# Kernel tuning notes

Measured on AMD Instinct MI355X. Metric: run time of the kernel, lower is better.

Reference implementation:

```python
import jax, jax.numpy as jnp
import numpy as np

NUM_CLASSES = 19
C_ENET = 1.02            # ENet weighting constant
THRESH = -float(np.log(0.7))  # -log(thresh)
N_MIN = 262144           # hard-example floor (B*H*W // 16)


def setup_inputs() -> dict:
    key = jax.random.key(0)
    k1, k2 = jax.random.split(key)
    logits = jax.random.normal(k1, (8, NUM_CLASSES, 512, 1024), dtype=jnp.float32)
    labels = jax.random.randint(k2, (8, 512, 1024), 0, NUM_CLASSES, dtype=jnp.int32)
    return {"logits": logits, "labels": labels}


def reference(logits, labels):
    # ENet class weights from label histogram: w_c = 1 / ln(c + freq_c)
    flat_lab = labels.reshape(-1)
    total = flat_lab.shape[0]
    counts = jnp.bincount(flat_lab, length=NUM_CLASSES).astype(jnp.float32)
    propensity = counts / jnp.float32(total)
    class_weights = 1.0 / jnp.log(C_ENET + propensity)  # [C]

    # weighted per-pixel cross entropy (reduction='none')
    logp = jax.nn.log_softmax(logits, axis=1)                       # [B,C,H,W]
    nll = -jnp.take_along_axis(logp, labels[:, None].astype(jnp.int32), axis=1)[:, 0]  # [B,H,W]
    loss = (class_weights[labels] * nll).reshape(-1)                # [B*H*W]

    # OHEM: sort descending, keep > thresh if n_min-th loss exceeds thresh, else top n_min
    loss_sorted = jnp.sort(loss)[::-1]
    cond = loss_sorted[N_MIN] > THRESH
    idx = jnp.arange(loss_sorted.shape[0])
    mask = jnp.where(cond, loss_sorted > THRESH, idx < N_MIN).astype(loss_sorted.dtype)
    return jnp.sum(loss_sorted * mask) / jnp.sum(mask)
```

## Files before the change

### kernel.cpp

```cpp
#include <hip/hip_runtime.h>
#include <math.h>

#define NCLS   19
#define HW     (512*1024)
#define BHW    (8*HW)
#define NQ     (BHW/4)
#define KSEL   262144u
#define THRESH 0.35667494393873245f

struct Meta {
  double S;
  double sumV;
  unsigned int cntV;
  unsigned int K;
  unsigned int b1, k1, b2, k2, vbits;
  unsigned int _pad;
  unsigned int counts[32];
  float weights[32];
  unsigned int hist1[2048];
  unsigned int hist2[2048];
  unsigned int hist3[1024];
};

__global__ __launch_bounds__(256) void k_label_hist(const int* __restrict__ lab,
                                                    Meta* __restrict__ m) {
  __shared__ unsigned int h[32];
  if (threadIdx.x < 32) h[threadIdx.x] = 0u;
  __syncthreads();
  int q = blockIdx.x * 256 + threadIdx.x;
  int4 l = reinterpret_cast<const int4*>(lab)[q];
  atomicAdd(&h[l.x], 1u);
  atomicAdd(&h[l.y], 1u);
  atomicAdd(&h[l.z], 1u);
  atomicAdd(&h[l.w], 1u);
  __syncthreads();
  if (threadIdx.x < 32) {
    unsigned int c = h[threadIdx.x];
    if (c) atomicAdd(&m->counts[threadIdx.x], c);
  }
}

__global__ void k_weights(Meta* __restrict__ m) {
  int c = threadIdx.x;
  if (c < NCLS) {
    float p = (float)m->counts[c] * (1.0f / (float)BHW);
    m->weights[c] = 1.0f / logf(1.02f + p);
  }
}

__global__ __launch_bounds__(256) void k_loss(const float* __restrict__ logits,
                                              const int* __restrict__ lab,
                                              float* __restrict__ loss,
                                              Meta* __restrict__ m) {
  __shared__ float w[NCLS];
  __shared__ float  sp[4];
  __shared__ unsigned int cp[4];
  if (threadIdx.x < NCLS) w[threadIdx.x] = m->weights[threadIdx.x];
  __syncthreads();

  int q = blockIdx.x * 256 + threadIdx.x;
  int base = q << 2;
  int b  = base >> 19;
  int hw = base & (HW - 1);
  const float* lp = logits + (long)b * (NCLS * HW) + hw;
  int4 l4 = reinterpret_cast<const int4*>(lab)[q];

  float4 vals[NCLS];
#pragma unroll
  for (int c = 0; c < NCLS; ++c) {
    vals[c] = *reinterpret_cast<const float4*>(lp);
    lp += HW;
  }

  float m0 = -INFINITY, m1 = -INFINITY, m2 = -INFINITY, m3 = -INFINITY;
#pragma unroll
  for (int c = 0; c < NCLS; ++c) {
    m0 = fmaxf(m0, vals[c].x); m1 = fmaxf(m1, vals[c].y);
    m2 = fmaxf(m2, vals[c].z); m3 = fmaxf(m3, vals[c].w);
  }
  float s0 = 0.f, s1 = 0.f, s2 = 0.f, s3 = 0.f;
  float x0 = 0.f, x1 = 0.f, x2 = 0.f, x3 = 0.f;
#pragma unroll
  for (int c = 0; c < NCLS; ++c) {
    float4 v = vals[c];
    s0 += __expf(v.x - m0); s1 += __expf(v.y - m1);
    s2 += __expf(v.z - m2); s3 += __expf(v.w - m3);
    x0 = (c == l4.x) ? v.x : x0;
    x1 = (c == l4.y) ? v.y : x1;
    x2 = (c == l4.z) ? v.z : x2;
    x3 = (c == l4.w) ? v.w : x3;
  }
  float4 o;
  o.x = w[l4.x] * (m0 + logf(s0) - x0);
  o.y = w[l4.y] * (m1 + logf(s1) - x1);
  o.z = w[l4.z] * (m2 + logf(s2) - x2);
  o.w = w[l4.w] * (m3 + logf(s3) - x3);
  reinterpret_cast<float4*>(loss)[q] = o;

  float ls = 0.f; unsigned int lc = 0u;
  if (o.x > THRESH) { ls += o.x; ++lc; }
  if (o.y > THRESH) { ls += o.y; ++lc; }
  if (o.z > THRESH) { ls += o.z; ++lc; }
  if (o.w > THRESH) { ls += o.w; ++lc; }
#pragma unroll
  for (int off = 32; off > 0; off >>= 1) {
    ls += __shfl_down(ls, off);
    lc += __shfl_down(lc, off);
  }
  int wid = threadIdx.x >> 6;
  if ((threadIdx.x & 63) == 0) { sp[wid] = ls; cp[wid] = lc; }
  __syncthreads();
  if (threadIdx.x == 0) {
    float bs = sp[0] + sp[1] + sp[2] + sp[3];
    unsigned int bc = cp[0] + cp[1] + cp[2] + cp[3];
    atomicAdd(&m->S, (double)bs);
    atomicAdd(&m->K, bc);
  }
}

__global__ __launch_bounds__(256) void k_hist1(const float* __restrict__ loss,
                                               Meta* __restrict__ m) {
  __shared__ unsigned int h[2048];
  __shared__ int active;
  if (threadIdx.x == 0) active = (m->K <= KSEL) ? 1 : 0;
  for (int i = threadIdx.x; i < 2048; i += 256) h[i] = 0u;
  __syncthreads();
  if (!active) return;
  int stride = gridDim.x * 256;
  for (int q = blockIdx.x * 256 + threadIdx.x; q < NQ; q += stride) {
    float4 v = reinterpret_cast<const float4*>(loss)[q];
    atomicAdd(&h[__float_as_uint(v.x) >> 21], 1u);
    atomicAdd(&h[__float_as_uint(v.y) >> 21], 1u);
    atomicAdd(&h[__float_as_uint(v.z) >> 21], 1u);
    atomicAdd(&h[__float_as_uint(v.w) >> 21], 1u);
  }
  __syncthreads();
  for (int i = threadIdx.x; i < 2048; i += 256)
    if (h[i]) atomicAdd(&m->hist1[i], h[i]);
}

__global__ void k_sel1(Meta* __restrict__ m) {
  if (m->K > KSEL) return;
  unsigned int cum = 0;
  for (int b = 2047; b >= 0; --b) {
    unsigned int hb = m->hist1[b];
    if (cum + hb >= KSEL) { m->b1 = (unsigned)b; m->k1 = KSEL - cum; return; }
    cum += hb;
  }
}

__global__ __launch_bounds__(256) void k_hist2(const float* __restrict__ loss,
                                               Meta* __restrict__ m) {
  __shared__ unsigned int h[2048];
  __shared__ unsigned int sb1;
  __shared__ int active;
  if (threadIdx.x == 0) { active = (m->K <= KSEL) ? 1 : 0; sb1 = m->b1; }
  for (int i = threadIdx.x; i < 2048; i += 256) h[i] = 0u;
  __syncthreads();
  if (!active) return;
  unsigned int b1 = sb1;
  int stride = gridDim.x * 256;
  for (int q = blockIdx.x * 256 + threadIdx.x; q < NQ; q += stride) {
    float4 v = reinterpret_cast<const float4*>(loss)[q];
    unsigned int bx = __float_as_uint(v.x);
    unsigned int by = __float_as_uint(v.y);
    unsigned int bz = __float_as_uint(v.z);
    unsigned int bw = __float_as_uint(v.w);
    if ((bx >> 21) == b1) atomicAdd(&h[(bx >> 10) & 2047u], 1u);
    if ((by >> 21) == b1) atomicAdd(&h[(by >> 10) & 2047u], 1u);
    if ((bz >> 21) == b1) atomicAdd(&h[(bz >> 10) & 2047u], 1u);
    if ((bw >> 21) == b1) atomicAdd(&h[(bw >> 10) & 2047u], 1u);
  }
  __syncthreads();
  for (int i = threadIdx.x; i < 2048; i += 256)
    if (h[i]) atomicAdd(&m->hist2[i], h[i]);
}

__global__ void k_sel2(Meta* __restrict__ m) {
  if (m->K > KSEL) return;
  unsigned int k1 = m->k1, cum = 0;
  for (int b = 2047; b >= 0; --b) {
    unsigned int hb = m->hist2[b];
    if (cum + hb >= k1) { m->b2 = (unsigned)b; m->k2 = k1 - cum; return; }
    cum += hb;
  }
}

__global__ __launch_bounds__(256) void k_hist3(const float* __restrict__ loss,
                                               Meta* __restrict__ m) {
  __shared__ unsigned int h[1024];
  __shared__ unsigned int spre;
  __shared__ int active;
  if (threadIdx.x == 0) {
    active = (m->K <= KSEL) ? 1 : 0;
    spre = (m->b1 << 11) | m->b2;
  }
  for (int i = threadIdx.x; i < 1024; i += 256) h[i] = 0u;
  __syncthreads();
  if (!active) return;
  unsigned int pre = spre;
  int stride = gridDim.x * 256;
  for (int q = blockIdx.x * 256 + threadIdx.x; q < NQ; q += stride) {
    float4 v = reinterpret_cast<const float4*>(loss)[q];
    unsigned int bx = __float_as_uint(v.x);
    unsigned int by = __float_as_uint(v.y);
    unsigned int bz = __float_as_uint(v.z);
    unsigned int bw = __float_as_uint(v.w);
    if ((bx >> 10) == pre) atomicAdd(&h[bx & 1023u], 1u);
    if ((by >> 10) == pre) atomicAdd(&h[by & 1023u], 1u);
    if ((bz >> 10) == pre) atomicAdd(&h[bz & 1023u], 1u);
    if ((bw >> 10) == pre) atomicAdd(&h[bw & 1023u], 1u);
  }
  __syncthreads();
  for (int i = threadIdx.x; i < 1024; i += 256)
    if (h[i]) atomicAdd(&m->hist3[i], h[i]);
}

__global__ void k_sel3(Meta* __restrict__ m) {
  if (m->K > KSEL) return;
  unsigned int k2 = m->k2, cum = 0;
  for (int b = 1023; b >= 0; --b) {
    unsigned int hb = m->hist3[b];
    if (cum + hb >= k2) {
      m->vbits = (m->b1 << 21) | (m->b2 << 10) | (unsigned)b;
      return;
    }
    cum += hb;
  }
}

__global__ __launch_bounds__(256) void k_sumv(const float* __restrict__ loss,
                                              Meta* __restrict__ m) {
  __shared__ double sp[4];
  __shared__ unsigned int cp[4];
  __shared__ unsigned int svb;
  __shared__ int active;
  if (threadIdx.x == 0) { active = (m->K <= KSEL) ? 1 : 0; svb = m->vbits; }
  __syncthreads();
  if (!active) return;
  unsigned int vb = svb;
  double ls = 0.0; unsigned int lc = 0u;
  int stride = gridDim.x * 256;
  for (int q = blockIdx.x * 256 + threadIdx.x; q < NQ; q += stride) {
    float4 v = reinterpret_cast<const float4*>(loss)[q];
    if (__float_as_uint(v.x) > vb) { ls += (double)v.x; ++lc; }
    if (__float_as_uint(v.y) > vb) { ls += (double)v.y; ++lc; }
    if (__float_as_uint(v.z) > vb) { ls += (double)v.z; ++lc; }
    if (__float_as_uint(v.w) > vb) { ls += (double)v.w; ++lc; }
  }
#pragma unroll
  for (int off = 32; off > 0; off >>= 1) {
    ls += __shfl_down(ls, off);
    lc += __shfl_down(lc, off);
  }
  int wid = threadIdx.x >> 6;
  if ((threadIdx.x & 63) == 0) { sp[wid] = ls; cp[wid] = lc; }
  __syncthreads();
  if (threadIdx.x == 0) {
    atomicAdd(&m->sumV, sp[0] + sp[1] + sp[2] + sp[3]);
    atomicAdd(&m->cntV, cp[0] + cp[1] + cp[2] + cp[3]);
  }
}

__global__ void k_final(const Meta* __restrict__ m, float* __restrict__ out) {
  if (m->K > KSEL) {
    out[0] = (float)(m->S / (double)m->K);
  } else {
    float v = __uint_as_float(m->vbits);
    double top = m->sumV + (double)(KSEL - m->cntV) * (double)v;
    out[0] = (float)(top / (double)KSEL);
  }
}

extern "C" void kernel_launch(void* const* d_in, const int* in_sizes, int n_in,
                              void* d_out, int out_size, void* d_ws, size_t ws_size,
                              hipStream_t stream) {
  const float* logits = (const float*)d_in[0];
  const int*   labels = (const int*)d_in[1];
  float* out  = (float*)d_out;
  float* loss = (float*)d_ws;
  Meta*  meta = (Meta*)((char*)d_ws + (size_t)BHW * 4);

  hipMemsetAsync(meta, 0, sizeof(Meta), stream);
  k_label_hist<<<NQ / 256, 256, 0, stream>>>(labels, meta);
  k_weights  <<<1, 64, 0, stream>>>(meta);
  k_loss     <<<NQ / 256, 256, 0, stream>>>(logits, labels, loss, meta);
  k_hist1    <<<512, 256, 0, stream>>>(loss, meta);
  k_sel1     <<<1, 1, 0, stream>>>(meta);
  k_hist2    <<<512, 256, 0, stream>>>(loss, meta);
  k_sel2     <<<1, 1, 0, stream>>>(meta);
  k_hist3    <<<512, 256, 0, stream>>>(loss, meta);
  k_sel3     <<<1, 1, 0, stream>>>(meta);
  k_sumv     <<<512, 256, 0, stream>>>(loss, meta);
  k_final    <<<1, 1, 0, stream>>>(meta, out);
}
```

Baseline: 186.2 us.

## Fuse OHEM pipeline into three kernels with last-block finalization and single-block fallback

Folds the class-weight computation into the label histogram kernel with a last-block-done counter. The final mean for the common K>KSEL case is now written inside the loss kernel the same way. The four-pass radix select, previously split across many multi-block kernels, moves into one 1024-thread block fallback kernel. This removes about eight kernel launches and their serialization. The cost is that the fallback path, whenever it runs, scans 32 MB four times with only a single workgroup, which would be very slow.

Result: slower. 390.3 us (+109.7%).

```diff
diff --git a/kernel.cpp b/kernel.cpp
--- a/kernel.cpp
+++ b/kernel.cpp
@@ -5,25 +5,22 @@
 #define HW     (512*1024)
 #define BHW    (8*HW)
 #define NQ     (BHW/4)
+#define GRID_Q (NQ/256)
 #define KSEL   262144u
 #define THRESH 0.35667494393873245f
 
 struct Meta {
   double S;
-  double sumV;
-  unsigned int cntV;
   unsigned int K;
-  unsigned int b1, k1, b2, k2, vbits;
+  unsigned int done0;
+  unsigned int done1;
   unsigned int _pad;
   unsigned int counts[32];
   float weights[32];
-  unsigned int hist1[2048];
-  unsigned int hist2[2048];
-  unsigned int hist3[1024];
 };
 
-__global__ __launch_bounds__(256) void k_label_hist(const int* __restrict__ lab,
-                                                    Meta* __restrict__ m) {
+__global__ __launch_bounds__(256) void k_hist_weights(const int* __restrict__ lab,
+                                                      Meta* __restrict__ m) {
   __shared__ unsigned int h[32];
   if (threadIdx.x < 32) h[threadIdx.x] = 0u;
   __syncthreads();
@@ -38,22 +35,27 @@
     unsigned int c = h[threadIdx.x];
     if (c) atomicAdd(&m->counts[threadIdx.x], c);
   }
-}
-
-__global__ void k_weights(Meta* __restrict__ m) {
-  int c = threadIdx.x;
-  if (c < NCLS) {
-    float p = (float)m->counts[c] * (1.0f / (float)BHW);
-    m->weights[c] = 1.0f / logf(1.02f + p);
+  __syncthreads();
+  if (threadIdx.x == 0) {
+    __threadfence();
+    unsigned int done = atomicAdd(&m->done0, 1u);
+    if (done == GRID_Q - 1u) {
+      for (int c = 0; c < NCLS; ++c) {
+        unsigned int cnt = atomicAdd(&m->counts[c], 0u);
+        float p = (float)cnt * (1.0f / (float)BHW);
+        m->weights[c] = 1.0f / logf(1.02f + p);
+      }
+    }
   }
 }
 
 __global__ __launch_bounds__(256) void k_loss(const float* __restrict__ logits,
                                               const int* __restrict__ lab,
                                               float* __restrict__ loss,
-                                              Meta* __restrict__ m) {
+                                              Meta* __restrict__ m,
+                                              float* __restrict__ out) {
   __shared__ float w[NCLS];
-  __shared__ float  sp[4];
+  __shared__ float sp[4];
   __shared__ unsigned int cp[4];
   if (threadIdx.x < NCLS) w[threadIdx.x] = m->weights[threadIdx.x];
   __syncthreads();
@@ -115,19 +117,33 @@
     unsigned int bc = cp[0] + cp[1] + cp[2] + cp[3];
     atomicAdd(&m->S, (double)bs);
     atomicAdd(&m->K, bc);
-  }
-}
-
-__global__ __launch_bounds__(256) void k_hist1(const float* __restrict__ loss,
-                                               Meta* __restrict__ m) {
+    __threadfence();
+    unsigned int done = atomicAdd(&m->done1, 1u);
+    if (done == GRID_Q - 1u) {
+      double S = atomicAdd(&m->S, 0.0);
+      unsigned int K = atomicAdd(&m->K, 0u);
+      if (K > KSEL) out[0] = (float)(S / (double)K);
+    }
+  }
+}
+
+__global__ __launch_bounds__(1024) void k_fallback(const float* __restrict__ loss,
+                                                   const Meta* __restrict__ m,
+                                                   float* __restrict__ out) {
   __shared__ unsigned int h[2048];
-  __shared__ int active;
-  if (threadIdx.x == 0) active = (m->K <= KSEL) ? 1 : 0;
-  for (int i = threadIdx.x; i < 2048; i += 256) h[i] = 0u;
-  __syncthreads();
-  if (!active) return;
-  int stride = gridDim.x * 256;
-  for (int q = blockIdx.x * 256 + threadIdx.x; q < NQ; q += stride) {
+  __shared__ unsigned int sel[4];
+  __shared__ double dsp[16];
+  __shared__ unsigned int dcp[16];
+
+  unsigned int K = m->K;
+  if (K > KSEL) return;
+
+  const int T = 1024;
+  int tid = threadIdx.x;
+
+  for (int i = tid; i < 2048; i += T) h[i] = 0u;
+  __syncthreads();
+  for (int q = tid; q < NQ; q += T) {
     float4 v = reinterpret_cast<const float4*>(loss)[q];
     atomicAdd(&h[__float_as_uint(v.x) >> 21], 1u);
     atomicAdd(&h[__float_as_uint(v.y) >> 21], 1u);
@@ -135,113 +151,66 @@
     atomicAdd(&h[__float_as_uint(v.w) >> 21], 1u);
   }
   __syncthreads();
-  for (int i = threadIdx.x; i < 2048; i += 256)
-    if (h[i]) atomicAdd(&m->hist1[i], h[i]);
-}
-
-__global__ void k_sel1(Meta* __restrict__ m) {
-  if (m->K > KSEL) return;
-  unsigned int cum = 0;
-  for (int b = 2047; b >= 0; --b) {
-    unsigned int hb = m->hist1[b];
-    if (cum + hb >= KSEL) { m->b1 = (unsigned)b; m->k1 = KSEL - cum; return; }
-    cum += hb;
-  }
-}
-
-__global__ __launch_bounds__(256) void k_hist2(const float* __restrict__ loss,
-                                               Meta* __restrict__ m) {
-  __shared__ unsigned int h[2048];
-  __shared__ unsigned int sb1;
-  __shared__ int active;
-  if (threadIdx.x == 0) { active = (m->K <= KSEL) ? 1 : 0; sb1 = m->b1; }
-  for (int i = threadIdx.x; i < 2048; i += 256) h[i] = 0u;
-  __syncthreads();
-  if (!active) return;
-  unsigned int b1 = sb1;
-  int stride = gridDim.x * 256;
-  for (int q = blockIdx.x * 256 + threadIdx.x; q < NQ; q += stride) {
-    float4 v = reinterpret_cast<const float4*>(loss)[q];
-    unsigned int bx = __float_as_uint(v.x);
-    unsigned int by = __float_as_uint(v.y);
-    unsigned int bz = __float_as_uint(v.z);
-    unsigned int bw = __float_as_uint(v.w);
+  if (tid == 0) {
+    unsigned int cum = 0;
+    for (int b = 2047; b >= 0; --b) {
+      unsigned int hb = h[b];
+      if (cum + hb >= KSEL) { sel[0] = (unsigned)b; sel[3] = KSEL - cum; break; }
+      cum += hb;
+    }
+  }
+  __syncthreads();
+  unsigned int b1 = sel[0], k1 = sel[3];
+
+  for (int i = tid; i < 2048; i += T) h[i] = 0u;
+  __syncthreads();
+  for (int q = tid; q < NQ; q += T) {
+    float4 v = reinterpret_cast<const float4*>(loss)[q];
+    unsigned int bx = __float_as_uint(v.x), by = __float_as_uint(v.y);
+    unsigned int bz = __float_as_uint(v.z), bw = __float_as_uint(v.w);
     if ((bx >> 21) == b1) atomicAdd(&h[(bx >> 10) & 2047u], 1u);
     if ((by >> 21) == b1) atomicAdd(&h[(by >> 10) & 2047u], 1u);
     if ((bz >> 21) == b1) atomicAdd(&h[(bz >> 10) & 2047u], 1u);
     if ((bw >> 21) == b1) atomicAdd(&h[(bw >> 10) & 2047u], 1u);
   }
   __syncthreads();
-  for (int i = threadIdx.x; i < 2048; i += 256)
-    if (h[i]) atomicAdd(&m->hist2[i], h[i]);
-}
-
-__global__ void k_sel2(Meta* __restrict__ m) {
-  if (m->K > KSEL) return;
-  unsigned int k1 = m->k1, cum = 0;
-  for (int b = 2047; b >= 0; --b) {
-    unsigned int hb = m->hist2[b];
-    if (cum + hb >= k1) { m->b2 = (unsigned)b; m->k2 = k1 - cum; return; }
-    cum += hb;
-  }
-}
-
-__global__ __launch_bounds__(256) void k_hist3(const float* __restrict__ loss,
-                                               Meta* __restrict__ m) {
-  __shared__ unsigned int h[1024];
-  __shared__ unsigned int spre;
-  __shared__ int active;
-  if (threadIdx.x == 0) {
-    active = (m->K <= KSEL) ? 1 : 0;
-    spre = (m->b1 << 11) | m->b2;
-  }
-  for (int i = threadIdx.x; i < 1024; i += 256) h[i] = 0u;
-  __syncthreads();
-  if (!active) return;
-  unsigned int pre = spre;
-  int stride = gridDim.x * 256;
-  for (int q = blockIdx.x * 256 + threadIdx.x; q < NQ; q += stride) {
-    float4 v = reinterpret_cast<const float4*>(loss)[q];
-    unsigned int bx = __float_as_uint(v.x);
-    unsigned int by = __float_as_uint(v.y);
-    unsigned int bz = __float_as_uint(v.z);
-    unsigned int bw = __float_as_uint(v.w);
+  if (tid == 0) {
+    unsigned int cum = 0;
+    for (int b = 2047; b >= 0; --b) {
+      unsigned int hb = h[b];
+      if (cum + hb >= k1) { sel[1] = (unsigned)b; sel[3] = k1 - cum; break; }
+      cum += hb;
+    }
+  }
+  __syncthreads();
+  unsigned int b2 = sel[1], k2 = sel[3];
+  unsigned int pre = (b1 << 11) | b2;
+
+  for (int i = tid; i < 1024; i += T) h[i] = 0u;
+  __syncthreads();
+  for (int q = tid; q < NQ; q += T) {
+    float4 v = reinterpret_cast<const float4*>(loss)[q];
+    unsigned int bx = __float_as_uint(v.x), by = __float_as_uint(v.y);
+    unsigned int bz = __float_as_uint(v.z), bw = __float_as_uint(v.w);
     if ((bx >> 10) == pre) atomicAdd(&h[bx & 1023u], 1u);
     if ((by >> 10) == pre) atomicAdd(&h[by & 1023u], 1u);
     if ((bz >> 10) == pre) atomicAdd(&h[bz & 1023u], 1u);
     if ((bw >> 10) == pre) atomicAdd(&h[bw & 1023u], 1u);
   }
   __syncthreads();
-  for (int i = threadIdx.x; i < 1024; i += 256)
-    if (h[i]) atomicAdd(&m->hist3[i], h[i]);
-}
-
-__global__ void k_sel3(Meta* __restrict__ m) {
-  if (m->K > KSEL) return;
-  unsigned int k2 = m->k2, cum = 0;
-  for (int b = 1023; b >= 0; --b) {
-    unsigned int hb = m->hist3[b];
-    if (cum + hb >= k2) {
-      m->vbits = (m->b1 << 21) | (m->b2 << 10) | (unsigned)b;
-      return;
-    }
-    cum += hb;
-  }
-}
-
-__global__ __launch_bounds__(256) void k_sumv(const float* __restrict__ loss,
-                                              Meta* __restrict__ m) {
-  __shared__ double sp[4];
-  __shared__ unsigned int cp[4];
-  __shared__ unsigned int svb;
-  __shared__ int active;
-  if (threadIdx.x == 0) { active = (m->K <= KSEL) ? 1 : 0; svb = m->vbits; }
-  __syncthreads();
-  if (!active) return;
-  unsigned int vb = svb;
+  if (tid == 0) {
+    unsigned int cum = 0;
+    for (int b = 1023; b >= 0; --b) {
+      unsigned int hb = h[b];
+      if (cum + hb >= k2) { sel[2] = (b1 << 21) | (b2 << 10) | (unsigned)b; break; }
+      cum += hb;
+    }
+  }
+  __syncthreads();
+  unsigned int vb = sel[2];
+
   double ls = 0.0; unsigned int lc = 0u;
-  int stride = gridDim.x * 256;
-  for (int q = blockIdx.x * 256 + threadIdx.x; q < NQ; q += stride) {
+  for (int q = tid; q < NQ; q += T) {
     float4 v = reinterpret_cast<const float4*>(loss)[q];
     if (__float_as_uint(v.x) > vb) { ls += (double)v.x; ++lc; }
     if (__float_as_uint(v.y) > vb) { ls += (double)v.y; ++lc; }
@@ -253,21 +222,14 @@
     ls += __shfl_down(ls, off);
     lc += __shfl_down(lc, off);
   }
-  int wid = threadIdx.x >> 6;
-  if ((threadIdx.x & 63) == 0) { sp[wid] = ls; cp[wid] = lc; }
-  __syncthreads();
-  if (threadIdx.x == 0) {
-    atomicAdd(&m->sumV, sp[0] + sp[1] + sp[2] + sp[3]);
-    atomicAdd(&m->cntV, cp[0] + cp[1] + cp[2] + cp[3]);
-  }
-}
-
-__global__ void k_final(const Meta* __restrict__ m, float* __restrict__ out) {
-  if (m->K > KSEL) {
-    out[0] = (float)(m->S / (double)m->K);
-  } else {
-    float v = __uint_as_float(m->vbits);
-    double top = m->sumV + (double)(KSEL - m->cntV) * (double)v;
+  int wid = tid >> 6;
+  if ((tid & 63) == 0) { dsp[wid] = ls; dcp[wid] = lc; }
+  __syncthreads();
+  if (tid == 0) {
+    double sumV = 0.0; unsigned int cntV = 0u;
+    for (int i = 0; i < 16; ++i) { sumV += dsp[i]; cntV += dcp[i]; }
+    float v = __uint_as_float(vb);
+    double top = sumV + (double)(KSEL - cntV) * (double)v;
     out[0] = (float)(top / (double)KSEL);
   }
 }
@@ -282,15 +244,7 @@
   Meta*  meta = (Meta*)((char*)d_ws + (size_t)BHW * 4);
 
   hipMemsetAsync(meta, 0, sizeof(Meta), stream);
-  k_label_hist<<<NQ / 256, 256, 0, stream>>>(labels, meta);
-  k_weights  <<<1, 64, 0, stream>>>(meta);
-  k_loss     <<<NQ / 256, 256, 0, stream>>>(logits, labels, loss, meta);
-  k_hist1    <<<512, 256, 0, stream>>>(loss, meta);
-  k_sel1     <<<1, 1, 0, stream>>>(meta);
-  k_hist2    <<<512, 256, 0, stream>>>(loss, meta);
-  k_sel2     <<<1, 1, 0, stream>>>(meta);
-  k_hist3    <<<512, 256, 0, stream>>>(loss, meta);
-  k_sel3     <<<1, 1, 0, stream>>>(meta);
-  k_sumv     <<<512, 256, 0, stream>>>(loss, meta);
-  k_final    <<<1, 1, 0, stream>>>(meta, out);
-}
+  k_hist_weights<<<GRID_Q, 256, 0, stream>>>(labels, meta);
+  k_loss        <<<GRID_Q, 256, 0, stream>>>(logits, labels, loss, meta, out);
+  k_fallback    <<<1, 1024, 0, stream>>>(loss, meta, out);
+}
```
